# Kernel optimization log

Measured on AMD Instinct MI355X. Metric: run time of the kernel, lower is better.

Reference implementation:

```python
import jax, jax.numpy as jnp
import numpy as np

B, S, HID = 2, 2048, 2048
H, KV, D = 32, 8, 64
GROUPS = H // KV
THETA = 10000.0
SCALE = D ** -0.5
NEG = -1e9


def setup_inputs() -> dict:
    key = jax.random.key(0)
    ks = jax.random.split(key, 5)
    x = jax.random.normal(ks[0], (B, S, 2 * HID), dtype=jnp.float32)
    # Linear weights stored as [in, out] (torch stores [out, in]; y = x @ W.T there)
    Wq = jax.random.normal(ks[1], (2 * HID, H * D), dtype=jnp.float32) * 0.02
    Wk = jax.random.normal(ks[2], (2 * HID, KV * D), dtype=jnp.float32) * 0.02
    Wv = jax.random.normal(ks[3], (2 * HID, KV * D), dtype=jnp.float32) * 0.02
    Wo = jax.random.normal(ks[4], (H * D, HID), dtype=jnp.float32) * 0.02
    # additive causal mask, broadcastable to [B, 1, S, S]
    causal = jnp.tril(jnp.ones((S, S), dtype=bool))
    attention_mask = jnp.where(causal, 0.0, NEG)[None, None].astype(jnp.float32)
    position_ids = jnp.broadcast_to(jnp.arange(S, dtype=jnp.int32)[None, :], (B, S))
    return {"combined_states": x, "attention_mask": attention_mask,
            "position_ids": position_ids, "Wq": Wq, "Wk": Wk, "Wv": Wv, "Wo": Wo}


def _rotate_half(x):
    x1, x2 = jnp.split(x, 2, axis=-1)
    return jnp.concatenate([-x2, x1], axis=-1)


def _rope_cos_sin(position_ids, dtype):
    inv_freq = 1.0 / (THETA ** (jnp.arange(0, D, 2, dtype=jnp.float32) / D))  # [D/2]
    freqs = position_ids.astype(jnp.float32)[..., None] * inv_freq  # [B, S, D/2]
    emb = jnp.concatenate([freqs, freqs], axis=-1)  # [B, S, D]
    return jnp.cos(emb).astype(dtype), jnp.sin(emb).astype(dtype)


def reference(combined_states, attention_mask, position_ids, Wq, Wk, Wv, Wo):
    x = combined_states
    q = (x @ Wq).reshape(B, S, H, D).transpose(0, 2, 1, 3)    # [B, H, S, D]
    k = (x @ Wk).reshape(B, S, KV, D).transpose(0, 2, 1, 3)   # [B, KV, S, D]
    v = (x @ Wv).reshape(B, S, KV, D).transpose(0, 2, 1, 3)
    cos, sin = _rope_cos_sin(position_ids, x.dtype)           # [B, S, D]
    cos, sin = cos[:, None], sin[:, None]                     # [B, 1, S, D]
    q = q * cos + _rotate_half(q) * sin
    k = k * cos + _rotate_half(k) * sin
    k = jnp.repeat(k, GROUPS, axis=1)                         # [B, H, S, D]
    v = jnp.repeat(v, GROUPS, axis=1)
    scores = jnp.einsum('bhqd,bhkd->bhqk', q, k) * SCALE + attention_mask
    probs = jax.nn.softmax(scores.astype(jnp.float32), axis=-1).astype(q.dtype)
    attn = jnp.einsum('bhqk,bhkd->bhqd', probs, v)            # [B, H, S, D]
    attn = attn.transpose(0, 2, 1, 3).reshape(B, S, H * D)
    return attn @ Wo
```

## Files before the change

### kernel.cpp

```cpp
#include <hip/hip_runtime.h>

#define S_LEN 2048
#define BATCH 2
#define HEADS 32
#define KVH   8
#define DH    64

typedef unsigned short u16;
typedef unsigned int   u32;
typedef u16   u16x8 __attribute__((ext_vector_type(8)));
typedef u16   u16x4 __attribute__((ext_vector_type(4)));
typedef short s16x8 __attribute__((ext_vector_type(8)));
typedef float f32x4 __attribute__((ext_vector_type(4)));
typedef u32   u32x2 __attribute__((ext_vector_type(2)));

__device__ __forceinline__ u16 f2bf(float f) {
    unsigned x; __builtin_memcpy(&x, &f, 4);
    x += 0x7fffu + ((x >> 16) & 1u);
    return (u16)(x >> 16);
}
__device__ __forceinline__ float bf2f(u16 u) {
    unsigned x = ((unsigned)u) << 16; float f; __builtin_memcpy(&f, &x, 4); return f;
}
__device__ __forceinline__ float fexp2(float x) {
#if __has_builtin(__builtin_amdgcn_exp2f)
    return __builtin_amdgcn_exp2f(x);
#else
    return exp2f(x);
#endif
}
__device__ __forceinline__ void gll16(const void* g, void* l) {
    __builtin_amdgcn_global_load_lds((const __attribute__((address_space(1))) unsigned*)g,
                                     (__attribute__((address_space(3))) unsigned*)l, 16, 0, 0);
}

__global__ __launch_bounds__(256) void k_f32_to_bf16(const float* __restrict__ src,
                                                     u16* __restrict__ dst, int n4) {
    int i = blockIdx.x * 256 + threadIdx.x;
    if (i < n4) {
        f32x4 v = ((const f32x4*)src)[i];
        u16x4 o;
        o.x = f2bf(v.x); o.y = f2bf(v.y); o.z = f2bf(v.z); o.w = f2bf(v.w);
        ((u16x4*)dst)[i] = o;
    }
}

__global__ __launch_bounds__(256) void k_wprep(const float* __restrict__ Wq, const float* __restrict__ Wk,
                                               const float* __restrict__ Wv, const float* __restrict__ Wo,
                                               u16* __restrict__ wqkvt, u16* __restrict__ wot) {
    __shared__ float t[32][33];
    int id = blockIdx.x;
    const float* src; u16* dst; int srcCols, dstStride, dstRowOff, bx, by;
    if (id < 8192)       { src = Wq; dst = wqkvt; srcCols = 2048; dstStride = 4096; dstRowOff = 0;    bx = id & 127; by = id >> 7; }
    else if (id < 10240) { id -= 8192;  src = Wk; dst = wqkvt; srcCols = 512; dstStride = 4096; dstRowOff = 2048; bx = id & 127; by = id >> 7; }
    else if (id < 12288) { id -= 10240; src = Wv; dst = wqkvt; srcCols = 512; dstStride = 4096; dstRowOff = 2560; bx = id & 127; by = id >> 7; }
    else                 { id -= 12288; src = Wo; dst = wot;   srcCols = 2048; dstStride = 2048; dstRowOff = 0;   bx = id & 63;  by = id >> 6; }
    int r0 = bx * 32, c0 = by * 32;
    int tx = threadIdx.x & 31, ty = threadIdx.x >> 5;
#pragma unroll
    for (int i = 0; i < 4; ++i)
        t[ty + 8 * i][tx] = src[(size_t)(r0 + ty + 8 * i) * srcCols + (c0 + tx)];
    __syncthreads();
#pragma unroll
    for (int i = 0; i < 4; ++i)
        dst[(size_t)(dstRowOff + c0 + ty + 8 * i) * dstStride + (r0 + tx)] = f2bf(t[tx][ty + 8 * i]);
}

template <int OUT_BF16>
__global__ __launch_bounds__(256) void k_gemm_bt(const u16* __restrict__ A,
                                                 const u16* __restrict__ Bt,
                                                 void* __restrict__ Cout,
                                                 int M, int N, int K) {
    __shared__ __align__(16) u16 As[8192];
    __shared__ __align__(16) u16 Bs[8192];
    int tid = threadIdx.x;
    int wave = tid >> 6, lane = tid & 63, m15 = lane & 15, quad = lane >> 4;
    int wm = (wave >> 1) * 64, wn = (wave & 1) * 64;

    int nwg = gridDim.x * gridDim.y;
    int bid = blockIdx.y * gridDim.x + blockIdx.x;
    if ((nwg & 7) == 0) bid = (bid & 7) * (nwg >> 3) + (bid >> 3);
    int bx = bid % gridDim.x, by = bid / gridDim.x;
    int m0 = by * 128, n0 = bx * 128;

    f32x4 acc[4][4];
#pragma unroll
    for (int i = 0; i < 4; ++i)
#pragma unroll
        for (int j = 0; j < 4; ++j) acc[i][j] = (f32x4){0.f, 0.f, 0.f, 0.f};

    int rl8 = lane >> 3;
    int sg8 = ((lane & 7) ^ rl8) * 8;
    const u16* Ag = A  + (size_t)(m0 + wave * 32 + rl8) * K + sg8;
    const u16* Bg = Bt + (size_t)(n0 + wave * 32 + rl8) * K + sg8;
    u16* Asl = As + (wave * 32) * 64;
    u16* Bsl = Bs + (wave * 32) * 64;
    int swq = m15 & 7;

    for (int k0 = 0; k0 < K; k0 += 64) {
        __syncthreads();
#pragma unroll
        for (int i = 0; i < 4; ++i) {
            gll16(Ag + (size_t)(8 * i) * K, Asl + (8 * i) * 64);
            gll16(Bg + (size_t)(8 * i) * K, Bsl + (8 * i) * 64);
        }
        Ag += 64; Bg += 64;
        __syncthreads();

#pragma unroll
        for (int kk = 0; kk < 2; ++kk) {
            int sgr = ((kk * 4 + quad) ^ swq) * 8;
            s16x8 af[4], bfr[4];
#pragma unroll
            for (int mt = 0; mt < 4; ++mt)
                af[mt] = *(const s16x8*)&As[(wm + mt * 16 + m15) * 64 + sgr];
#pragma unroll
            for (int nt = 0; nt < 4; ++nt)
                bfr[nt] = *(const s16x8*)&Bs[(wn + nt * 16 + m15) * 64 + sgr];
#pragma unroll
            for (int mt = 0; mt < 4; ++mt)
#pragma unroll
                for (int nt = 0; nt < 4; ++nt)
                    acc[mt][nt] = __builtin_amdgcn_mfma_f32_16x16x32_bf16(af[mt], bfr[nt], acc[mt][nt], 0, 0, 0);
        }
    }

#pragma unroll
    for (int mt = 0; mt < 4; ++mt)
#pragma unroll
        for (int nt = 0; nt < 4; ++nt)
#pragma unroll
            for (int r = 0; r < 4; ++r) {
                size_t row = m0 + wm + mt * 16 + quad * 4 + r;
                size_t col = n0 + wn + nt * 16 + m15;
                float v = acc[mt][nt][r];
                if (OUT_BF16) ((u16*)Cout)[row * N + col] = f2bf(v);
                else          ((float*)Cout)[row * N + col] = v;
            }
}

__global__ __launch_bounds__(512, 2) void k_gemm8p(const u16* __restrict__ A,
                                                   const u16* __restrict__ Bt,
                                                   u16* __restrict__ Cout,
                                                   int M, int N, int K) {
    __shared__ __align__(16) u16 Ls[8][8192];
    const int tid = threadIdx.x;
    const int wave = tid >> 6, lane = tid & 63;
    const int m15 = lane & 15, quad = lane >> 4;
    const int wm = wave >> 2, wn = wave & 3;
    const int rl8 = lane >> 3;
    const int sg8 = ((lane & 7) ^ rl8) * 8;
    const int m0 = blockIdx.y * 256, n0 = blockIdx.x * 256;

    const u16* Abase = A  + (size_t)(m0 + wave * 16 + rl8) * K + sg8;
    const u16* Bbase = Bt + (size_t)(n0 + wave * 16 + rl8) * K + sg8;
    u16* Lst = &Ls[0][0] + wave * 1024;
    const int aro = (wm * 16 + m15) * 64;
    const int bro = (wn * 16 + m15) * 64;
    const int sx = m15 & 7;

    f32x4 acc[8][4];
#pragma unroll
    for (int i = 0; i < 8; ++i)
#pragma unroll
        for (int j = 0; j < 4; ++j) acc[i][j] = (f32x4){0.f, 0.f, 0.f, 0.f};
    s16x8 rA0a[8], rA1a[8], rA0b[8], rA1b[8];
    s16x8 rB0a[4], rB1a[4], rB0b[4], rB1b[4];

#define STG8(slot, c, t) do { \
    const u16* gsrc_ = ((c) & 1) ? Abase : Bbase; \
    size_t off_ = (size_t)(((c) >> 1) * 128) * K + (size_t)(t) * 64; \
    u16* ld_ = Lst + (slot) * 8192; \
    gll16(gsrc_ + off_, ld_); \
    gll16(gsrc_ + off_ + (size_t)8 * K, ld_ + 512); \
} while (0)

#define RDA8(slot, rg) do { \
    const u16* sb_ = &Ls[slot][0] + aro; \
    _Pragma("unroll") \
    for (int mt_ = 0; mt_ < 4; ++mt_) \
        _Pragma("unroll") \
        for (int kk_ = 0; kk_ < 2; ++kk_) \
            rg[mt_ * 2 + kk_] = *(const s16x8*)&sb_[mt_ * 2048 + (((kk_ * 4 + quad) ^ sx) * 8)]; \
} while (0)

#define RDB8(slot, rg) do { \
    const u16* sb_ = &Ls[slot][0] + bro; \
    _Pragma("unroll") \
    for (int nt_ = 0; nt_ < 2; ++nt_) \
        _Pragma("unroll") \
        for (int kk_ = 0; kk_ < 2; ++kk_) \
            rg[nt_ * 2 + kk_] = *(const s16x8*)&sb_[nt_ * 4096 + (((kk_ * 4 + quad) ^ sx) * 8)]; \
} while (0)

#define MM8(ra, rb, mi, ni) do { \
    _Pragma("unroll") \
    for (int mt_ = 0; mt_ < 4; ++mt_) \
        _Pragma("unroll") \
        for (int nt_ = 0; nt_ < 2; ++nt_) \
            _Pragma("unroll") \
            for (int kk_ = 0; kk_ < 2; ++kk_) \
                acc[(mi) + mt_][(ni) + nt_] = __builtin_amdgcn_mfma_f32_16x16x32_bf16( \
                    ra[mt_ * 2 + kk_], rb[nt_ * 2 + kk_], acc[(mi) + mt_][(ni) + nt_], 0, 0, 0); \
} while (0)

#define BAR8() asm volatile("s_barrier" ::: "memory")
#define LGKM8() do { asm volatile("s_waitcnt lgkmcnt(0)" ::: "memory"); \
                     __builtin_amdgcn_sched_barrier(0); } while (0)
#define GUARD8(more) do { \
    if (more) asm volatile("s_waitcnt vmcnt(6)" ::: "memory"); \
    else      asm volatile("s_waitcnt vmcnt(0)" ::: "memory"); \
} while (0)

    const int NT2 = K >> 7;

    STG8(0, 0, 0); STG8(1, 1, 0); STG8(2, 2, 0); STG8(3, 3, 0);
    STG8(4, 0, 1); STG8(5, 1, 1); STG8(6, 2, 1);
    asm volatile("s_waitcnt vmcnt(6)" ::: "memory");
    BAR8();
    RDB8(0, rB0a);

    for (int it = 0; it < NT2; ++it) {
        const int t2 = 2 * it + 2, t3 = 2 * it + 3;
        const bool more = (it < NT2 - 1);

        STG8(7, 3, 2 * it + 1);
        BAR8(); LGKM8();
        __builtin_amdgcn_s_setprio(1);
        if (it) MM8(rA1b, rB1b, 4, 2);
        RDA8(1, rA0a);
        __builtin_amdgcn_s_setprio(0);
        BAR8();
        if (more) STG8(0, 0, t2);
        BAR8(); LGKM8();
        __builtin_amdgcn_s_setprio(1);
        MM8(rA0a, rB0a, 0, 0);
        RDB8(2, rB1a);
        __builtin_amdgcn_s_setprio(0);
        BAR8();
        if (more) STG8(1, 1, t2);
        BAR8(); LGKM8();
        __builtin_amdgcn_s_setprio(1);
        MM8(rA0a, rB1a, 0, 2);
        RDA8(3, rA1a);
        __builtin_amdgcn_s_setprio(0);
        BAR8();
        if (more) STG8(2, 2, t2);
        BAR8(); LGKM8();
        GUARD8(more);
        __builtin_amdgcn_s_setprio(1);
        MM8(rA1a, rB0a, 4, 0);
        RDB8(4, rB0b);
        __builtin_amdgcn_s_setprio(0);
        BAR8();
        if (more) STG8(3, 3, t2);
        BAR8(); LGKM8();
        __builtin_amdgcn_s_setprio(1);
        MM8(rA1a, rB1a, 4, 2);
        RDA8(5, rA0b);
        __builtin_amdgcn_s_setprio(0);
        BAR8();
        if (more) STG8(4, 0, t3);
        BAR8(); LGKM8();
        __builtin_amdgcn_s_setprio(1);
        MM8(rA0b, rB0b, 0, 0);
        RDB8(6, rB1b);
        __builtin_amdgcn_s_setprio(0);
        BAR8();
        if (more) STG8(5, 1, t3);
        BAR8(); LGKM8();
        __builtin_amdgcn_s_setprio(1);
        MM8(rA0b, rB1b, 0, 2);
        RDA8(7, rA1b);
        __builtin_amdgcn_s_setprio(0);
        BAR8();
        if (more) STG8(6, 2, t3);
        BAR8(); LGKM8();
        GUARD8(more);
        __builtin_amdgcn_s_setprio(1);
        MM8(rA1b, rB0b, 4, 0);
        if (more) RDB8(0, rB0a);
        __builtin_amdgcn_s_setprio(0);
        BAR8();
    }
    MM8(rA1b, rB1b, 4, 2);

#pragma unroll
    for (int i = 0; i < 8; ++i) {
        size_t row = (size_t)(m0 + (i & 3) * 32 + wm * 16 + (i >> 2) * 128 + quad * 4);
#pragma unroll
        for (int j = 0; j < 4; ++j) {
            size_t col = (size_t)(n0 + (j & 1) * 64 + wn * 16 + (j >> 1) * 128 + m15);
#pragma unroll
            for (int r = 0; r < 4; ++r)
                Cout[(row + r) * N + col] = f2bf(acc[i][j][r]);
        }
    }
#undef STG8
#undef RDA8
#undef RDB8
#undef MM8
#undef BAR8
#undef LGKM8
#undef GUARD8
}

__global__ __launch_bounds__(256) void k_vtrans(const u16* __restrict__ qkv, u16* __restrict__ vt) {
    __shared__ u16 t[64][72];
    int s0 = blockIdx.x * 64;
    int bkv = blockIdx.y;
    int tid = threadIdx.x;
    int row = tid >> 2, seg = tid & 3;
    int b = bkv >> 3, kv = bkv & 7;
    const u16* src = qkv + (size_t)(b * S_LEN + s0 + row) * 3072 + 2560 + kv * 64 + seg * 16;
    *(u16x8*)&t[row][seg * 16]     = *(const u16x8*)(src);
    *(u16x8*)&t[row][seg * 16 + 8] = *(const u16x8*)(src + 8);
    __syncthreads();
    int d = tid >> 2, sseg = tid & 3;
    u16x8 o0, o1;
#pragma unroll
    for (int j = 0; j < 8; ++j) {
        o0[j] = t[(j & 3) * 16 + sseg * 4 + (j >> 2)][d];
        o1[j] = t[(j & 3) * 16 + sseg * 4 + (j >> 2) + 2][d];
    }
    u16* dst = vt + ((size_t)bkv * 64 + d) * S_LEN + s0 + sseg * 16;
    *(u16x8*)(dst)     = o0;
    *(u16x8*)(dst + 8) = o1;
}

__global__ __launch_bounds__(256) void k_rope(const u16* __restrict__ qkv,
                                              const int* __restrict__ pos_ids,
                                              u16* __restrict__ qo, u16* __restrict__ ko) {
    int bs = blockIdx.x;
    int b = bs >> 11, s = bs & 2047;
    int tid = threadIdx.x;
    float pos = (float)pos_ids[bs];
    const u16* row = qkv + (size_t)bs * 3072;

#pragma unroll
    for (int p = tid; p < 1024; p += 256) {
        int h = p >> 5, i = p & 31;
        float inv = fexp2((float)i * -0.4152410119f);
        float ang = pos * inv;
        float sn, c; __sincosf(ang, &sn, &c);
        float a = bf2f(row[h * 64 + i]);
        float bq = bf2f(row[h * 64 + i + 32]);
        size_t base = ((size_t)(b * HEADS + h) * S_LEN + s) * DH;
        qo[base + i]      = f2bf(a * c - bq * sn);
        qo[base + i + 32] = f2bf(bq * c + a * sn);
    }
    {
        int p = tid;
        if (p < 256) {
            int kv = p >> 5, i = p & 31;
            float inv = fexp2((float)i * -0.4152410119f);
            float ang = pos * inv;
            float sn, c; __sincosf(ang, &sn, &c);
            float a = bf2f(row[2048 + kv * 64 + i]);
            float bk = bf2f(row[2048 + kv * 64 + i + 32]);
            size_t base = ((size_t)(b * KVH + kv) * S_LEN + s) * DH;
            ko[base + i]      = f2bf(a * c - bk * sn);
            ko[base + i + 32] = f2bf(bk * c + a * sn);
        }
    }
}

__global__ __launch_bounds__(256) void k_attn(const u16* __restrict__ q, const u16* __restrict__ k,
                                              const u16* __restrict__ vt, u16* __restrict__ out) {
    __shared__ __align__(16) u16 Qs[4096];
    __shared__ __align__(16) u16 Ks[8192];
    __shared__ __align__(16) u16 Vts[8192];
    __shared__ __align__(16) u16 Ps[4 * 16 * 72];
    int bh = blockIdx.y;
    int b = bh >> 5, h = bh & 31, kvh = h >> 2;
    int tid = threadIdx.x, wave = tid >> 6, lane = tid & 63, m15 = lane & 15, quad = lane >> 4;

    const u16* qhb = q + (size_t)(b * HEADS + h) * S_LEN * DH;
    const u16* kb  = k + (size_t)(b * KVH + kvh) * S_LEN * DH;
    const u16* vb  = vt + (size_t)(b * KVH + kvh) * DH * S_LEN;
    u16* PsW = &Ps[wave * 16 * 72];
    const float C = 0.1803368801f;

    int rl8 = lane >> 3;
    int sg8 = ((lane & 7) ^ rl8) * 8;
    int swq = m15 & 7;
    int vrow = lane >> 4;
    int vgrp = lane & 15;

    for (int half = 0; half < 2; ++half) {
        int jt = half ? (31 - (int)blockIdx.x) : (int)blockIdx.x;
        int q0 = jt * 64;
        __syncthreads();
        {
            const u16* qg = qhb + (size_t)(q0 + wave * 16 + rl8) * DH + sg8;
            gll16(qg,          Qs + (wave * 16) * 64);
            gll16(qg + 8 * DH, Qs + (wave * 16 + 8) * 64);
        }

        float lsum[4];
        f32x4 oacc[4];
#pragma unroll
        for (int r = 0; r < 4; ++r) lsum[r] = 0.f;
#pragma unroll
        for (int dt = 0; dt < 4; ++dt) oacc[dt] = (f32x4){0.f, 0.f, 0.f, 0.f};

        for (int ib = 0; ib <= jt; ib += 2) {
            int kk0 = ib * 64;
            int nsub = (jt - ib >= 1) ? 2 : 1;
            __syncthreads();
            {
                const u16* kg = kb + (size_t)(kk0 + wave * 32 + rl8) * DH + sg8;
#pragma unroll
                for (int i = 0; i < 4; ++i)
                    gll16(kg + (size_t)(8 * i) * DH, Ks + (wave * 32 + 8 * i) * 64);
#pragma unroll
                for (int i = 0; i < 4; ++i) {
                    int d = wave * 16 + 4 * i + vrow;
                    const u16* vg = vb + (size_t)d * S_LEN + kk0 + ((vgrp ^ (d & 7)) * 8);
                    gll16(vg, Vts + (wave * 16 + 4 * i) * 128);
                }
            }
            __syncthreads();

            for (int sub = 0; sub < nsub; ++sub) {
                f32x4 sacc[4];
#pragma unroll
                for (int nt = 0; nt < 4; ++nt) sacc[nt] = (f32x4){0.f, 0.f, 0.f, 0.f};
#pragma unroll
                for (int kk = 0; kk < 2; ++kk) {
                    int sgr = ((kk * 4 + quad) ^ swq) * 8;
                    s16x8 aF = *(const s16x8*)&Qs[(wave * 16 + m15) * 64 + sgr];
#pragma unroll
                    for (int nt = 0; nt < 4; ++nt) {
                        s16x8 bF = *(const s16x8*)&Ks[(sub * 64 + nt * 16 + m15) * 64 + sgr];
                        sacc[nt] = __builtin_amdgcn_mfma_f32_16x16x32_bf16(aF, bF, sacc[nt], 0, 0, 0);
                    }
                }

                bool dsub = (kk0 + sub * 64) == q0;
#pragma unroll
                for (int r = 0; r < 4; ++r) {
                    int qrr = wave * 16 + quad * 4 + r;
                    float p0[4];
#pragma unroll
                    for (int nt = 0; nt < 4; ++nt) {
                        float s2 = sacc[nt][r] * C - 12.0f;
                        if (dsub && (nt * 16 + m15 > qrr)) s2 = -1e30f;
                        p0[nt] = fexp2(s2);
                        lsum[r] += p0[nt];
                    }
                    unsigned a0, a1, a2, a3;
                    __builtin_memcpy(&a0, &p0[0], 4); __builtin_memcpy(&a1, &p0[1], 4);
                    __builtin_memcpy(&a2, &p0[2], 4); __builtin_memcpy(&a3, &p0[3], 4);
                    u32x2 w;
                    w.x = (a0 >> 16) | (a1 & 0xffff0000u);
                    w.y = (a2 >> 16) | (a3 & 0xffff0000u);
                    *(u32x2*)&PsW[(quad * 4 + r) * 72 + m15 * 4] = w;
                }

#pragma unroll
                for (int kk = 0; kk < 2; ++kk) {
                    s16x8 aF = *(const s16x8*)&PsW[m15 * 72 + kk * 32 + quad * 8];
                    int g = (sub * 8 + kk * 4 + quad) ^ swq;
#pragma unroll
                    for (int dt = 0; dt < 4; ++dt) {
                        s16x8 bF = *(const s16x8*)&Vts[(dt * 16 + m15) * 128 + g * 8];
                        oacc[dt] = __builtin_amdgcn_mfma_f32_16x16x32_bf16(aF, bF, oacc[dt], 0, 0, 0);
                    }
                }
            }
        }

#pragma unroll
        for (int r = 0; r < 4; ++r) {
            float ls = lsum[r];
#pragma unroll
            for (int off = 1; off < 16; off <<= 1) ls += __shfl_xor(ls, off, 64);
            float inv = 1.f / ls;
            int qrow = q0 + wave * 16 + quad * 4 + r;
#pragma unroll
            for (int dt = 0; dt < 4; ++dt)
                out[((size_t)(b * S_LEN) + qrow) * (size_t)(HEADS * DH) + h * DH + dt * 16 + m15] =
                    f2bf(oacc[dt][r] * inv);
        }
    }
}

extern "C" void kernel_launch(void* const* d_in, const int* in_sizes, int n_in,
                              void* d_out, int out_size, void* d_ws, size_t ws_size,
                              hipStream_t stream) {
    const float* x  = (const float*)d_in[0];
    const int*   pos = (const int*)d_in[2];
    const float* Wq = (const float*)d_in[3];
    const float* Wk = (const float*)d_in[4];
    const float* Wv = (const float*)d_in[5];
    const float* Wo = (const float*)d_in[6];

    char* ws = (char*)d_ws;
    const size_t NEED = 92274688;
    if (ws_size < NEED) return;

    u16* xbf   = (u16*)(ws);
    u16* vt    = (u16*)(ws + 16777216);
    u16* wqkvt = (u16*)(ws + 33554432);
    u16* wot   = (u16*)(ws + 58720256);
    u16* qkv   = (u16*)(ws + 67108864);
    u16* qro   = wqkvt;
    u16* kro   = qro + 8388608;
    u16* attn  = xbf;

    k_f32_to_bf16<<<16384, 256, 0, stream>>>(x, xbf, 4194304);
    k_wprep<<<16384, 256, 0, stream>>>(Wq, Wk, Wv, Wo, wqkvt, wot);
    { dim3 g(12, 16); k_gemm8p<<<g, 512, 0, stream>>>(xbf, wqkvt, qkv, 4096, 3072, 4096); }
    { dim3 g(32, 16); k_vtrans<<<g, 256, 0, stream>>>(qkv, vt); }
    k_rope<<<4096, 256, 0, stream>>>(qkv, pos, qro, kro);
    { dim3 g(16, 64); k_attn<<<g, 256, 0, stream>>>(qro, kro, vt, attn); }
    { dim3 g(16, 32); k_gemm_bt<0><<<g, 256, 0, stream>>>(attn, wot, (float*)d_out, 4096, 2048, 2048); }
}
```

Baseline: 399.2 us.

## Double-buffer K/V tiles in attention to overlap loads with MFMA compute

Replaces the single 128-key K/V shared-memory tile with two 64-key buffers. The next tile is prefetched into the alternate buffer while the current one is consumed, and the barrier count drops to one per tile. This aims to hide global-to-LDS load latency behind the QK and PV MFMAs. The trade-off is twice as many loop iterations for the same keys, and correctness depends on the async LDS loads having completed by the next barrier.

Result: no change. 398.2 us (-0.3%).

```diff
diff --git a/kernel.cpp b/kernel.cpp
--- a/kernel.cpp
+++ b/kernel.cpp
@@ -368,8 +368,8 @@
 __global__ __launch_bounds__(256) void k_attn(const u16* __restrict__ q, const u16* __restrict__ k,
                                               const u16* __restrict__ vt, u16* __restrict__ out) {
     __shared__ __align__(16) u16 Qs[4096];
-    __shared__ __align__(16) u16 Ks[8192];
-    __shared__ __align__(16) u16 Vts[8192];
+    __shared__ __align__(16) u16 Ks[2][4096];
+    __shared__ __align__(16) u16 Vts[2][4096];
     __shared__ __align__(16) u16 Ps[4 * 16 * 72];
     int bh = blockIdx.y;
     int b = bh >> 5, h = bh & 31, kvh = h >> 2;
@@ -384,8 +384,20 @@
     int rl8 = lane >> 3;
     int sg8 = ((lane & 7) ^ rl8) * 8;
     int swq = m15 & 7;
-    int vrow = lane >> 4;
-    int vgrp = lane & 15;
+    int vrow = lane >> 3;
+    int vgrp = lane & 7;
+
+#define STAGE_KV(bf, kk0) do { \
+    const u16* kg_ = kb + (size_t)((kk0) + wave * 16 + rl8) * DH + sg8; \
+    gll16(kg_,               &Ks[bf][(wave * 16) * 64]); \
+    gll16(kg_ + 8 * DH,      &Ks[bf][(wave * 16 + 8) * 64]); \
+    _Pragma("unroll") \
+    for (int i_ = 0; i_ < 2; ++i_) { \
+        int d_ = wave * 16 + 8 * i_ + vrow; \
+        const u16* vg_ = vb + (size_t)d_ * S_LEN + (kk0) + ((vgrp ^ (d_ & 7)) * 8); \
+        gll16(vg_, &Vts[bf][(wave * 16 + 8 * i_) * 64]); \
+    } \
+} while (0)
 
     for (int half = 0; half < 2; ++half) {
         int jt = half ? (31 - (int)blockIdx.x) : (int)blockIdx.x;
@@ -396,6 +408,7 @@
             gll16(qg,          Qs + (wave * 16) * 64);
             gll16(qg + 8 * DH, Qs + (wave * 16 + 8) * 64);
         }
+        STAGE_KV(0, 0);
 
         float lsum[4];
         f32x4 oacc[4];
@@ -404,69 +417,54 @@
 #pragma unroll
         for (int dt = 0; dt < 4; ++dt) oacc[dt] = (f32x4){0.f, 0.f, 0.f, 0.f};
 
-        for (int ib = 0; ib <= jt; ib += 2) {
-            int kk0 = ib * 64;
-            int nsub = (jt - ib >= 1) ? 2 : 1;
+        for (int ib = 0; ib <= jt; ++ib) {
+            int cur = ib & 1;
             __syncthreads();
-            {
-                const u16* kg = kb + (size_t)(kk0 + wave * 32 + rl8) * DH + sg8;
-#pragma unroll
-                for (int i = 0; i < 4; ++i)
-                    gll16(kg + (size_t)(8 * i) * DH, Ks + (wave * 32 + 8 * i) * 64);
-#pragma unroll
-                for (int i = 0; i < 4; ++i) {
-                    int d = wave * 16 + 4 * i + vrow;
-                    const u16* vg = vb + (size_t)d * S_LEN + kk0 + ((vgrp ^ (d & 7)) * 8);
-                    gll16(vg, Vts + (wave * 16 + 4 * i) * 128);
+            if (ib < jt) STAGE_KV(cur ^ 1, (ib + 1) * 64);
+
+            f32x4 sacc[4];
+#pragma unroll
+            for (int nt = 0; nt < 4; ++nt) sacc[nt] = (f32x4){0.f, 0.f, 0.f, 0.f};
+#pragma unroll
+            for (int kk = 0; kk < 2; ++kk) {
+                int sgr = ((kk * 4 + quad) ^ swq) * 8;
+                s16x8 aF = *(const s16x8*)&Qs[(wave * 16 + m15) * 64 + sgr];
+#pragma unroll
+                for (int nt = 0; nt < 4; ++nt) {
+                    s16x8 bF = *(const s16x8*)&Ks[cur][(nt * 16 + m15) * 64 + sgr];
+                    sacc[nt] = __builtin_amdgcn_mfma_f32_16x16x32_bf16(aF, bF, sacc[nt], 0, 0, 0);
                 }
             }
-            __syncthreads();
-
-            for (int sub = 0; sub < nsub; ++sub) {
-                f32x4 sacc[4];
-#pragma unroll
-                for (int nt = 0; nt < 4; ++nt) sacc[nt] = (f32x4){0.f, 0.f, 0.f, 0.f};
-#pragma unroll
-                for (int kk = 0; kk < 2; ++kk) {
-                    int sgr = ((kk * 4 + quad) ^ swq) * 8;
-                    s16x8 aF = *(const s16x8*)&Qs[(wave * 16 + m15) * 64 + sgr];
-#pragma unroll
-                    for (int nt = 0; nt < 4; ++nt) {
-                        s16x8 bF = *(const s16x8*)&Ks[(sub * 64 + nt * 16 + m15) * 64 + sgr];
-                        sacc[nt] = __builtin_amdgcn_mfma_f32_16x16x32_bf16(aF, bF, sacc[nt], 0, 0, 0);
-                    }
+
+            bool dsub = (ib == jt);
+#pragma unroll
+            for (int r = 0; r < 4; ++r) {
+                int qrr = wave * 16 + quad * 4 + r;
+                float p0[4];
+#pragma unroll
+                for (int nt = 0; nt < 4; ++nt) {
+                    float s2 = sacc[nt][r] * C - 12.0f;
+                    if (dsub && (nt * 16 + m15 > qrr)) s2 = -1e30f;
+                    p0[nt] = fexp2(s2);
+                    lsum[r] += p0[nt];
                 }
-
-                bool dsub = (kk0 + sub * 64) == q0;
-#pragma unroll
-                for (int r = 0; r < 4; ++r) {
-                    int qrr = wave * 16 + quad * 4 + r;
-                    float p0[4];
-#pragma unroll
-                    for (int nt = 0; nt < 4; ++nt) {
-                        float s2 = sacc[nt][r] * C - 12.0f;
-                        if (dsub && (nt * 16 + m15 > qrr)) s2 = -1e30f;
-                        p0[nt] = fexp2(s2);
-                        lsum[r] += p0[nt];
-                    }
-                    unsigned a0, a1, a2, a3;
-                    __builtin_memcpy(&a0, &p0[0], 4); __builtin_memcpy(&a1, &p0[1], 4);
-                    __builtin_memcpy(&a2, &p0[2], 4); __builtin_memcpy(&a3, &p0[3], 4);
-                    u32x2 w;
-                    w.x = (a0 >> 16) | (a1 & 0xffff0000u);
-                    w.y = (a2 >> 16) | (a3 & 0xffff0000u);
-                    *(u32x2*)&PsW[(quad * 4 + r) * 72 + m15 * 4] = w;
-                }
-
-#pragma unroll
-                for (int kk = 0; kk < 2; ++kk) {
-                    s16x8 aF = *(const s16x8*)&PsW[m15 * 72 + kk * 32 + quad * 8];
-                    int g = (sub * 8 + kk * 4 + quad) ^ swq;
-#pragma unroll
-                    for (int dt = 0; dt < 4; ++dt) {
-                        s16x8 bF = *(const s16x8*)&Vts[(dt * 16 + m15) * 128 + g * 8];
-                        oacc[dt] = __builtin_amdgcn_mfma_f32_16x16x32_bf16(aF, bF, oacc[dt], 0, 0, 0);
-                    }
+                unsigned a0, a1, a2, a3;
+                __builtin_memcpy(&a0, &p0[0], 4); __builtin_memcpy(&a1, &p0[1], 4);
+                __builtin_memcpy(&a2, &p0[2], 4); __builtin_memcpy(&a3, &p0[3], 4);
+                u32x2 w;
+                w.x = (a0 >> 16) | (a1 & 0xffff0000u);
+                w.y = (a2 >> 16) | (a3 & 0xffff0000u);
+                *(u32x2*)&PsW[(quad * 4 + r) * 72 + m15 * 4] = w;
+            }
+
+#pragma unroll
+            for (int kk = 0; kk < 2; ++kk) {
+                s16x8 aF = *(const s16x8*)&PsW[m15 * 72 + kk * 32 + quad * 8];
+                int g = (kk * 4 + quad) ^ swq;
+#pragma unroll
+                for (int dt = 0; dt < 4; ++dt) {
+                    s16x8 bF = *(const s16x8*)&Vts[cur][(dt * 16 + m15) * 64 + g * 8];
+                    oacc[dt] = __builtin_amdgcn_mfma_f32_16x16x32_bf16(aF, bF, oacc[dt], 0, 0, 0);
                 }
             }
         }
@@ -484,6 +482,7 @@
                     f2bf(oacc[dt][r] * inv);
         }
     }
+#undef STAGE_KV
 }
 
 extern "C" void kernel_launch(void* const* d_in, const int* in_sizes, int n_in,
```
